# Kernel optimization log

Hardware: AMD Instinct MI355X
Metric: run time of the kernel (lower is better)

Reference implementation:

```python
import jax, jax.numpy as jnp
import numpy as np

B, N, C = 2, 2048, 768
H = 12
D = C // H
WINDOW = 129  # odd; half-window = 64
SCALE = D ** -0.5


def setup_inputs() -> dict:
    key = jax.random.key(0)
    k_x, k_qkv, k_proj, k_pb = jax.random.split(key, 4)
    x = jax.random.normal(k_x, (B, N, C), dtype=jnp.float32)
    # nn.Linear weights: stored as [out, in]; qkv_bias=False so no qkv bias
    w_qkv = jax.random.normal(k_qkv, (3 * C, C), dtype=jnp.float32) * (C ** -0.5)
    w_proj = jax.random.normal(k_proj, (C, C), dtype=jnp.float32) * (C ** -0.5)
    b_proj = jax.random.normal(k_pb, (C,), dtype=jnp.float32) * 0.01
    return {"x": x, "w_qkv": w_qkv, "w_proj": w_proj, "b_proj": b_proj}


def reference(x, w_qkv, w_proj, b_proj):
    b, n, c = x.shape
    # qkv projection: [B,N,3C] -> [3,B,H,N,D]
    qkv = jnp.einsum('bnc,ec->bne', x, w_qkv)
    qkv = qkv.reshape(b, n, 3, H, D).transpose(2, 0, 3, 1, 4)
    q, k, v = qkv[0], qkv[1], qkv[2]
    # dense scores then sliding-window mask (faithful to source)
    attn = jnp.einsum('bhnd,bhmd->bhnm', q, k) * SCALE
    half = WINDOW // 2
    idx = jnp.arange(n)
    mask = jnp.abs(idx[:, None] - idx[None, :]) <= half  # [N,N]
    attn = jnp.where(mask[None, None], attn, -jnp.inf)
    attn = jax.nn.softmax(attn, axis=-1)
    attn = jnp.nan_to_num(attn)
    out = jnp.einsum('bhnm,bhmd->bhnd', attn, v)  # [B,H,N,D]
    out = out.transpose(0, 2, 1, 3).reshape(b, n, c)
    out = jnp.einsum('bnc,oc->bno', out, w_proj) + b_proj
    return out
```

## Files before the change

### kernel.cpp

```cpp
#include <hip/hip_runtime.h>
#include <hip/hip_bf16.h>

#define Bsz   2
#define Nseq  2048
#define Cdim  768
#define E3    2304
#define Hh    12
#define Dd    64
#define HALF  64
#define SCALEF 0.125f

typedef __attribute__((ext_vector_type(8))) short short8;
typedef __attribute__((ext_vector_type(4))) float f32x4;

__device__ __forceinline__ unsigned short f2bf(float f) {
    unsigned int u = __float_as_uint(f);
    u = (u + 0x7FFFu + ((u >> 16) & 1u)) >> 16;
    return (unsigned short)u;
}
__device__ __forceinline__ unsigned int pk2(float a, float b) {
    __hip_bfloat162 h = __float22bfloat162_rn(make_float2(a, b));
    union { __hip_bfloat162 h2; unsigned int u; } cv; cv.h2 = h; return cv.u;
}
__device__ __forceinline__ uint4 cvt8(const float4& lo, const float4& hi) {
    return make_uint4(pk2(lo.x, lo.y), pk2(lo.z, lo.w),
                      pk2(hi.x, hi.y), pk2(hi.z, hi.w));
}

__device__ __forceinline__ void gl_lds16(const unsigned short* g, unsigned short* l) {
    __builtin_amdgcn_global_load_lds(
        (__attribute__((address_space(1))) void*)(g),
        (__attribute__((address_space(3))) void*)(l), 16, 0, 0);
}

#define AST 72

__global__ __launch_bounds__(256) void cvt3(
    const float* __restrict__ x, const float* __restrict__ wq,
    const float* __restrict__ wp, unsigned short* __restrict__ xb,
    unsigned short* __restrict__ wqb, unsigned short* __restrict__ wpb)
{
    const int gid = blockIdx.x * 256 + threadIdx.x;
    const float* src; unsigned short* dst; int off;
    if (gid < 393216)      { src = x;  dst = xb;  off = gid; }
    else if (gid < 614400) { src = wq; dst = wqb; off = gid - 393216; }
    else                   { src = wp; dst = wpb; off = gid - 614400; }
    const float4 lo = *(const float4*)&src[(size_t)off * 8];
    const float4 hi = *(const float4*)&src[(size_t)off * 8 + 4];
    *(uint4*)&dst[(size_t)off * 8] = cvt8(lo, hi);
}

__global__ __launch_bounds__(256) void qkv_mfma(
    const unsigned short* __restrict__ xb, const unsigned short* __restrict__ wqb,
    unsigned short* __restrict__ qkvb)
{
    __shared__ __align__(16) unsigned short smem[12288];
    unsigned short* Asm = smem;
    unsigned short* Bsm = smem + 8192;

    const int t  = threadIdx.x;
    const int id = blockIdx.y * 36 + blockIdx.x;
    const int p8 = id & 7, jb2 = id >> 3;
    const int bx = (p8 & 3) * 9 + (jb2 % 9);
    const int by = (p8 >> 2) * 16 + (jb2 / 9);
    const int row0 = by * 128, col0 = bx * 64;

    const int lane = t & 63, wave = t >> 6;
    const int wm = wave >> 1, wn = wave & 1;
    const int ln = lane & 15, quad = lane >> 4;
    const int lr  = lane >> 3;
    const int sc  = ((lane ^ lr) & 7) * 8;
    const int xsw = (ln & 7) << 3;

    f32x4 acc[4][2] = {};

    for (int k0 = 0; k0 < Cdim; k0 += 64) {
        __syncthreads();
#pragma unroll
        for (int j = 0; j < 4; ++j)
            gl_lds16(&xb[(size_t)(row0 + wave*32 + j*8 + lr) * Cdim + k0 + sc],
                     &Asm[(wave*4 + j) * 512]);
#pragma unroll
        for (int j = 0; j < 2; ++j)
            gl_lds16(&wqb[(size_t)(col0 + wave*16 + j*8 + lr) * Cdim + k0 + sc],
                     &Bsm[(wave*2 + j) * 512]);
        __syncthreads();
#pragma unroll
        for (int kk = 0; kk < 2; ++kk) {
            short8 af[4], bf[2];
#pragma unroll
            for (int mi = 0; mi < 4; ++mi)
                af[mi] = *(const short8*)&Asm[(wm*64 + mi*16 + ln)*64
                                              + ((kk*32 + quad*8) ^ xsw)];
#pragma unroll
            for (int ni = 0; ni < 2; ++ni)
                bf[ni] = *(const short8*)&Bsm[(wn*32 + ni*16 + ln)*64
                                              + ((kk*32 + quad*8) ^ xsw)];
#pragma unroll
            for (int mi = 0; mi < 4; ++mi)
#pragma unroll
                for (int ni = 0; ni < 2; ++ni)
                    acc[mi][ni] = __builtin_amdgcn_mfma_f32_16x16x32_bf16(
                        af[mi], bf[ni], acc[mi][ni], 0, 0, 0);
        }
    }

    __syncthreads();
    unsigned short (*Cs)[AST] = (unsigned short(*)[AST])smem;
    const int rA = t >> 3, c8 = t & 7;
#pragma unroll
    for (int mi = 0; mi < 4; ++mi)
#pragma unroll
        for (int ni = 0; ni < 2; ++ni)
#pragma unroll
            for (int reg = 0; reg < 4; ++reg)
                Cs[wm*64 + mi*16 + quad*4 + reg][wn*32 + ni*16 + ln] =
                    f2bf(acc[mi][ni][reg]);
    __syncthreads();
#pragma unroll
    for (int j = 0; j < 4; ++j)
        *(uint4*)&qkvb[(size_t)(row0 + rA + j*32) * E3 + col0 + c8*8] =
            *(const uint4*)&Cs[rA + j*32][c8*8];
}

__global__ __launch_bounds__(256) void proj_mfma(
    const unsigned short* __restrict__ Ab, const unsigned short* __restrict__ wpb,
    const float* __restrict__ bias, float* __restrict__ out)
{
    __shared__ __align__(16) unsigned short smem[8192];
    unsigned short* Asm = smem;
    unsigned short* Bsm = smem + 4096;

    const int t  = threadIdx.x;
    const int id = blockIdx.y * 12 + blockIdx.x;
    const int p8 = id & 7, j2 = id >> 3;
    const int bx = j2 % 12;
    const int by = p8 * 8 + j2 / 12;
    const int row0 = by * 64, col0 = bx * 64;

    const int lane = t & 63, wave = t >> 6;
    const int ln = lane & 15, quad = lane >> 4;
    const int lr  = lane >> 3;
    const int sc  = ((lane ^ lr) & 7) * 8;
    const int xsw = (ln & 7) << 3;

    f32x4 acc[4] = {};

    for (int k0 = 0; k0 < Cdim; k0 += 64) {
        __syncthreads();
#pragma unroll
        for (int j = 0; j < 2; ++j) {
            const int r = wave*16 + j*8 + lr;
            gl_lds16(&Ab[(size_t)(row0 + r) * Cdim + k0 + sc],
                     &Asm[(wave*2 + j) * 512]);
            gl_lds16(&wpb[(size_t)(col0 + r) * Cdim + k0 + sc],
                     &Bsm[(wave*2 + j) * 512]);
        }
        __syncthreads();
#pragma unroll
        for (int kc = 0; kc < 2; ++kc) {
            short8 af = *(const short8*)&Asm[(wave*16 + ln)*64
                                             + ((kc*32 + quad*8) ^ xsw)];
#pragma unroll
            for (int ni = 0; ni < 4; ++ni) {
                short8 bf = *(const short8*)&Bsm[(ni*16 + ln)*64
                                                 + ((kc*32 + quad*8) ^ xsw)];
                acc[ni] = __builtin_amdgcn_mfma_f32_16x16x32_bf16(af, bf, acc[ni], 0, 0, 0);
            }
        }
    }

    float (*Csf)[36] = (float(*)[36])smem;
#pragma unroll
    for (int p = 0; p < 2; ++p) {
        __syncthreads();
#pragma unroll
        for (int ni = 0; ni < 2; ++ni) {
            const int nn = p * 2 + ni;
#pragma unroll
            for (int reg = 0; reg < 4; ++reg)
                Csf[wave*16 + quad*4 + reg][ni*16 + ln] = acc[nn][reg];
        }
        __syncthreads();
#pragma unroll
        for (int j = 0; j < 2; ++j) {
            const int F = t + j * 256, r = F >> 3, c4 = F & 7;
            const int col = col0 + p * 32 + c4 * 4;
            float4 v  = *(const float4*)&Csf[r][c4 * 4];
            float4 bv = *(const float4*)&bias[col];
            *(float4*)&out[(size_t)(row0 + r) * Cdim + col] =
                make_float4(v.x + bv.x, v.y + bv.y, v.z + bv.z, v.w + bv.w);
        }
    }
}

#define TQ   32
#define ROWS 160
#define KST  72
#define VST  168

__global__ __launch_bounds__(256) void swin_attn(
    const unsigned short* __restrict__ qkvb, unsigned short* __restrict__ ab)
{
    __shared__ __align__(16) unsigned short SH[ROWS * KST];
    __shared__ __align__(16) unsigned short Pl[TQ][VST];
    __shared__ float pmax[4][TQ];
    __shared__ float psum[4][TQ];
    unsigned short (*Ks)[KST] = (unsigned short(*)[KST])SH;
    unsigned short (*Vt)[VST] = (unsigned short(*)[VST])SH;

    const int t  = threadIdx.x;
    const int bh = blockIdx.y;
    const int b  = bh / Hh, h = bh % Hh;
    const int i0 = blockIdx.x * TQ;
    const int hoff = h * Dd;

    const int lane = t & 63, wave = t >> 6;
    const int ln = lane & 15, quad = lane >> 4;
    const int mi    = wave & 1;
    const int khalf = wave >> 1;

    short8 qf[2];
#pragma unroll
    for (int kc = 0; kc < 2; ++kc)
        qf[kc] = *(const short8*)&qkvb[(size_t)(b * Nseq + i0 + mi*16 + ln) * E3
                                       + hoff + kc*32 + quad*8];
    uint4 vreg[5];
    const int rV = t >> 3, c8 = t & 7;
#pragma unroll
    for (int j = 0; j < 5; ++j) {
        const int r = rV + j * 32;
        const int g = i0 - HALF + r;
        uint4 v = make_uint4(0u, 0u, 0u, 0u);
        if (g >= 0 && g < Nseq)
            v = *(const uint4*)&qkvb[(size_t)(b * Nseq + g) * E3 + 2*Cdim + hoff + c8*8];
        vreg[j] = v;
    }
#pragma unroll
    for (int j = 0; j < 5; ++j) {
        const int r = rV + j * 32;
        const int g = i0 - HALF + r;
        uint4 v = make_uint4(0u, 0u, 0u, 0u);
        if (g >= 0 && g < Nseq)
            v = *(const uint4*)&qkvb[(size_t)(b * Nseq + g) * E3 + Cdim + hoff + c8*8];
        *(uint4*)&Ks[r][c8 * 8] = v;
    }
    __syncthreads();

    f32x4 sacc[5] = {};
#pragma unroll
    for (int kc = 0; kc < 2; ++kc)
#pragma unroll
        for (int tt = 0; tt < 5; ++tt) {
            short8 kf = *(const short8*)&Ks[(khalf*5 + tt)*16 + ln][kc*32 + quad*8];
            sacc[tt] = __builtin_amdgcn_mfma_f32_16x16x32_bf16(qf[kc], kf, sacc[tt], 0, 0, 0);
        }

    float p[5][4];
    float pm[4] = {-1e30f, -1e30f, -1e30f, -1e30f};
#pragma unroll
    for (int tt = 0; tt < 5; ++tt) {
        const int j = (khalf*5 + tt)*16 + ln;
        const int g = i0 - HALF + j;
#pragma unroll
        for (int reg = 0; reg < 4; ++reg) {
            const int q = mi*16 + quad*4 + reg;
            const bool valid = (j >= q) && (j <= q + 2*HALF) && (g >= 0) && (g < Nseq);
            const float s = valid ? sacc[tt][reg] * SCALEF : -1e30f;
            p[tt][reg] = s;
            pm[reg] = fmaxf(pm[reg], s);
        }
    }
#pragma unroll
    for (int reg = 0; reg < 4; ++reg) {
        pm[reg] = fmaxf(pm[reg], __shfl_xor(pm[reg], 1));
        pm[reg] = fmaxf(pm[reg], __shfl_xor(pm[reg], 2));
        pm[reg] = fmaxf(pm[reg], __shfl_xor(pm[reg], 4));
        pm[reg] = fmaxf(pm[reg], __shfl_xor(pm[reg], 8));
    }
    if (ln == 0)
#pragma unroll
        for (int reg = 0; reg < 4; ++reg)
            pmax[wave][mi*16 + quad*4 + reg] = pm[reg];
    __syncthreads();

    float ps[4] = {};
#pragma unroll
    for (int reg = 0; reg < 4; ++reg) {
        const int q = mi*16 + quad*4 + reg;
        const float cm = fmaxf(pmax[mi][q], pmax[mi | 2][q]);
#pragma unroll
        for (int tt = 0; tt < 5; ++tt) {
            const float pv = (p[tt][reg] > -1e29f) ? __expf(p[tt][reg] - cm) : 0.f;
            p[tt][reg] = pv;
            ps[reg] += pv;
        }
    }
#pragma unroll
    for (int reg = 0; reg < 4; ++reg) {
        ps[reg] += __shfl_xor(ps[reg], 1);
        ps[reg] += __shfl_xor(ps[reg], 2);
        ps[reg] += __shfl_xor(ps[reg], 4);
        ps[reg] += __shfl_xor(ps[reg], 8);
    }
    if (ln == 0)
#pragma unroll
        for (int reg = 0; reg < 4; ++reg)
            psum[wave][mi*16 + quad*4 + reg] = ps[reg];
#pragma unroll
    for (int tt = 0; tt < 5; ++tt)
#pragma unroll
        for (int reg = 0; reg < 4; ++reg)
            Pl[mi*16 + quad*4 + reg][(khalf*5 + tt)*16 + ln] = f2bf(p[tt][reg]);
#pragma unroll
    for (int j = 0; j < 5; ++j) {
        const int r = rV + j * 32;
        union { unsigned short us[8]; uint4 u; } pk; pk.u = vreg[j];
#pragma unroll
        for (int jj = 0; jj < 8; ++jj)
            Vt[c8 * 8 + jj][r] = pk.us[jj];
    }
    __syncthreads();

    const int niq = wave & 1;
    const int mb  = (wave >> 1) * 2;
    f32x4 oacc[2] = {};
#pragma unroll
    for (int kc = 0; kc < 5; ++kc) {
        short8 pf = *(const short8*)&Pl[niq*16 + ln][kc*32 + quad*8];
#pragma unroll
        for (int m2 = 0; m2 < 2; ++m2) {
            short8 vf = *(const short8*)&Vt[(mb + m2)*16 + ln][kc*32 + quad*8];
            oacc[m2] = __builtin_amdgcn_mfma_f32_16x16x32_bf16(vf, pf, oacc[m2], 0, 0, 0);
        }
    }

    const int q = niq*16 + ln;
    const float inv = 1.f / (psum[q >> 4][q] + psum[(q >> 4) | 2][q]);
    unsigned short* orow = &ab[(size_t)(b * Nseq + i0 + q) * Cdim + hoff];
#pragma unroll
    for (int m2 = 0; m2 < 2; ++m2) {
        const int d0 = (mb + m2)*16 + quad*4;
        union { unsigned short us[4]; uint2 u2; } pk;
#pragma unroll
        for (int reg = 0; reg < 4; ++reg)
            pk.us[reg] = f2bf(oacc[m2][reg] * inv);
        *(uint2*)&orow[d0] = pk.u2;
    }
}

extern "C" void kernel_launch(void* const* d_in, const int* in_sizes, int n_in,
                              void* d_out, int out_size, void* d_ws, size_t ws_size,
                              hipStream_t stream)
{
    const float* x      = (const float*)d_in[0];
    const float* w_qkv  = (const float*)d_in[1];
    const float* w_proj = (const float*)d_in[2];
    const float* b_proj = (const float*)d_in[3];
    float* out = (float*)d_out;

    unsigned short* qkvb = (unsigned short*)d_ws;
    unsigned short* ab   = qkvb + 9437184;
    unsigned short* xb   = ab   + 3145728;
    unsigned short* wqb  = xb   + 3145728;
    unsigned short* wpb  = wqb  + 1769472;

    cvt3<<<dim3(2688), 256, 0, stream>>>(x, w_qkv, w_proj, xb, wqb, wpb);
    qkv_mfma<<<dim3(36, 32), 256, 0, stream>>>(xb, wqb, qkvb);
    swin_attn<<<dim3(Nseq / TQ, Bsz * Hh), 256, 0, stream>>>(qkvb, ab);
    proj_mfma<<<dim3(12, 64), 256, 0, stream>>>(ab, wpb, b_proj, out);
}
```

Before: 131.4 us.

## Widen QKV GEMM tiles and swizzle attention K/V shared-memory layouts

The QKV GEMM now uses 128x128 output tiles instead of 128x64, doubling per-wave MFMA work and halving the grid, with a two-pass bf16 epilogue through LDS. The attention kernel loads K straight into LDS with async global_load_lds and an XOR-swizzled layout, clamping out-of-range rows instead of zero-filling. It also stores the transposed V with an XOR swizzle to reduce bank conflicts, and remaps block IDs for L2 locality. The larger GEMM tile costs more registers and leaves fewer blocks (576), which may reduce occupancy.

```diff
diff --git a/kernel.cpp b/kernel.cpp
--- a/kernel.cpp
+++ b/kernel.cpp
@@ -33,8 +33,6 @@
         (__attribute__((address_space(3))) void*)(l), 16, 0, 0);
 }
 
-#define AST 72
-
 __global__ __launch_bounds__(256) void cvt3(
     const float* __restrict__ x, const float* __restrict__ wq,
     const float* __restrict__ wp, unsigned short* __restrict__ xb,
@@ -54,16 +52,16 @@
     const unsigned short* __restrict__ xb, const unsigned short* __restrict__ wqb,
     unsigned short* __restrict__ qkvb)
 {
-    __shared__ __align__(16) unsigned short smem[12288];
+    __shared__ __align__(16) unsigned short smem[16384];
     unsigned short* Asm = smem;
     unsigned short* Bsm = smem + 8192;
 
     const int t  = threadIdx.x;
-    const int id = blockIdx.y * 36 + blockIdx.x;
-    const int p8 = id & 7, jb2 = id >> 3;
-    const int bx = (p8 & 3) * 9 + (jb2 % 9);
-    const int by = (p8 >> 2) * 16 + (jb2 / 9);
-    const int row0 = by * 128, col0 = bx * 64;
+    const int id = blockIdx.y * 18 + blockIdx.x;
+    const int p8 = id & 7, j8 = id >> 3;
+    const int wg = p8 * 72 + j8;
+    const int by = wg / 18, bx = wg % 18;
+    const int row0 = by * 128, col0 = bx * 128;
 
     const int lane = t & 63, wave = t >> 6;
     const int wm = wave >> 1, wn = wave & 1;
@@ -72,55 +70,59 @@
     const int sc  = ((lane ^ lr) & 7) * 8;
     const int xsw = (ln & 7) << 3;
 
-    f32x4 acc[4][2] = {};
+    f32x4 acc[4][4] = {};
 
     for (int k0 = 0; k0 < Cdim; k0 += 64) {
         __syncthreads();
 #pragma unroll
-        for (int j = 0; j < 4; ++j)
+        for (int j = 0; j < 4; ++j) {
             gl_lds16(&xb[(size_t)(row0 + wave*32 + j*8 + lr) * Cdim + k0 + sc],
                      &Asm[(wave*4 + j) * 512]);
-#pragma unroll
-        for (int j = 0; j < 2; ++j)
-            gl_lds16(&wqb[(size_t)(col0 + wave*16 + j*8 + lr) * Cdim + k0 + sc],
-                     &Bsm[(wave*2 + j) * 512]);
+            gl_lds16(&wqb[(size_t)(col0 + wave*32 + j*8 + lr) * Cdim + k0 + sc],
+                     &Bsm[(wave*4 + j) * 512]);
+        }
         __syncthreads();
 #pragma unroll
         for (int kk = 0; kk < 2; ++kk) {
-            short8 af[4], bf[2];
+            short8 af[4], bf[4];
 #pragma unroll
             for (int mi = 0; mi < 4; ++mi)
                 af[mi] = *(const short8*)&Asm[(wm*64 + mi*16 + ln)*64
                                               + ((kk*32 + quad*8) ^ xsw)];
 #pragma unroll
-            for (int ni = 0; ni < 2; ++ni)
-                bf[ni] = *(const short8*)&Bsm[(wn*32 + ni*16 + ln)*64
+            for (int ni = 0; ni < 4; ++ni)
+                bf[ni] = *(const short8*)&Bsm[(wn*64 + ni*16 + ln)*64
                                               + ((kk*32 + quad*8) ^ xsw)];
 #pragma unroll
             for (int mi = 0; mi < 4; ++mi)
 #pragma unroll
-                for (int ni = 0; ni < 2; ++ni)
+                for (int ni = 0; ni < 4; ++ni)
                     acc[mi][ni] = __builtin_amdgcn_mfma_f32_16x16x32_bf16(
                         af[mi], bf[ni], acc[mi][ni], 0, 0, 0);
         }
     }
 
-    __syncthreads();
-    unsigned short (*Cs)[AST] = (unsigned short(*)[AST])smem;
+    unsigned short (*Cs)[72] = (unsigned short(*)[72])smem;
     const int rA = t >> 3, c8 = t & 7;
 #pragma unroll
-    for (int mi = 0; mi < 4; ++mi)
-#pragma unroll
-        for (int ni = 0; ni < 2; ++ni)
-#pragma unroll
-            for (int reg = 0; reg < 4; ++reg)
-                Cs[wm*64 + mi*16 + quad*4 + reg][wn*32 + ni*16 + ln] =
-                    f2bf(acc[mi][ni][reg]);
-    __syncthreads();
-#pragma unroll
-    for (int j = 0; j < 4; ++j)
-        *(uint4*)&qkvb[(size_t)(row0 + rA + j*32) * E3 + col0 + c8*8] =
-            *(const uint4*)&Cs[rA + j*32][c8*8];
+    for (int p = 0; p < 2; ++p) {
+        __syncthreads();
+        if (wn == p) {
+#pragma unroll
+            for (int mi = 0; mi < 4; ++mi)
+#pragma unroll
+                for (int ni = 0; ni < 4; ++ni)
+#pragma unroll
+                    for (int reg = 0; reg < 4; ++reg)
+                        Cs[wm*64 + mi*16 + quad*4 + reg][ni*16 + ln] =
+                            f2bf(acc[mi][ni][reg]);
+        }
+        __syncthreads();
+#pragma unroll
+        for (int j = 0; j < 4; ++j)
+            *(uint4*)&qkvb[(size_t)(row0 + rA + j*32) * E3 + col0 + p*64 + c8*8] =
+                *(const uint4*)&Cs[rA + j*32][c8*8];
+    }
 }
 
 __global__ __launch_bounds__(256) void proj_mfma(
@@ -196,29 +198,32 @@
 
 #define TQ   32
 #define ROWS 160
-#define KST  72
-#define VST  168
+#define VSTn 200
+#define PST  168
 
 __global__ __launch_bounds__(256) void swin_attn(
     const unsigned short* __restrict__ qkvb, unsigned short* __restrict__ ab)
 {
-    __shared__ __align__(16) unsigned short SH[ROWS * KST];
-    __shared__ __align__(16) unsigned short Pl[TQ][VST];
+    __shared__ __align__(16) unsigned short SH[64 * VSTn];
+    __shared__ __align__(16) unsigned short Pl[TQ][PST];
     __shared__ float pmax[4][TQ];
     __shared__ float psum[4][TQ];
-    unsigned short (*Ks)[KST] = (unsigned short(*)[KST])SH;
-    unsigned short (*Vt)[VST] = (unsigned short(*)[VST])SH;
 
     const int t  = threadIdx.x;
-    const int bh = blockIdx.y;
+    const int n  = blockIdx.y * 64 + blockIdx.x;
+    const int p8 = n & 7, jj8 = n >> 3;
+    const int bh = jj8 >> 3;
+    const int i0 = (p8 * 8 + (jj8 & 7)) * TQ;
     const int b  = bh / Hh, h = bh % Hh;
-    const int i0 = blockIdx.x * TQ;
     const int hoff = h * Dd;
 
     const int lane = t & 63, wave = t >> 6;
     const int ln = lane & 15, quad = lane >> 4;
     const int mi    = wave & 1;
     const int khalf = wave >> 1;
+    const int lr   = lane >> 3;
+    const int scw  = ((lane ^ lr) & 7) * 8;
+    const int xsw  = (ln & 7) << 3;
 
     short8 qf[2];
 #pragma unroll
@@ -238,12 +243,11 @@
     }
 #pragma unroll
     for (int j = 0; j < 5; ++j) {
-        const int r = rV + j * 32;
-        const int g = i0 - HALF + r;
-        uint4 v = make_uint4(0u, 0u, 0u, 0u);
-        if (g >= 0 && g < Nseq)
-            v = *(const uint4*)&qkvb[(size_t)(b * Nseq + g) * E3 + Cdim + hoff + c8*8];
-        *(uint4*)&Ks[r][c8 * 8] = v;
+        const int base = j * 32 + wave * 8;
+        int g = i0 - HALF + base + lr;
+        g = min(max(g, 0), Nseq - 1);
+        gl_lds16(&qkvb[(size_t)(b * Nseq + g) * E3 + Cdim + hoff + scw],
+                 &SH[base * 64]);
     }
     __syncthreads();
 
@@ -252,7 +256,8 @@
     for (int kc = 0; kc < 2; ++kc)
 #pragma unroll
         for (int tt = 0; tt < 5; ++tt) {
-            short8 kf = *(const short8*)&Ks[(khalf*5 + tt)*16 + ln][kc*32 + quad*8];
+            short8 kf = *(const short8*)&SH[((khalf*5 + tt)*16 + ln)*64
+                                            + ((kc*32 + quad*8) ^ xsw)];
             sacc[tt] = __builtin_amdgcn_mfma_f32_16x16x32_bf16(qf[kc], kf, sacc[tt], 0, 0, 0);
         }
 
@@ -315,10 +320,11 @@
 #pragma unroll
     for (int j = 0; j < 5; ++j) {
         const int r = rV + j * 32;
+        const int gr = ((r >> 3) ^ c8) * 8 + (r & 7);
         union { unsigned short us[8]; uint4 u; } pk; pk.u = vreg[j];
 #pragma unroll
-        for (int jj = 0; jj < 8; ++jj)
-            Vt[c8 * 8 + jj][r] = pk.us[jj];
+        for (int d8 = 0; d8 < 8; ++d8)
+            SH[(c8 * 8 + d8) * VSTn + gr] = pk.us[d8];
     }
     __syncthreads();
 
@@ -330,7 +336,9 @@
         short8 pf = *(const short8*)&Pl[niq*16 + ln][kc*32 + quad*8];
 #pragma unroll
         for (int m2 = 0; m2 < 2; ++m2) {
-            short8 vf = *(const short8*)&Vt[(mb + m2)*16 + ln][kc*32 + quad*8];
+            const int d = (mb + m2)*16 + ln;
+            short8 vf = *(const short8*)&SH[d * VSTn
+                                            + (((kc*4 + quad) ^ (d >> 3)) << 3)];
             oacc[m2] = __builtin_amdgcn_mfma_f32_16x16x32_bf16(vf, pf, oacc[m2], 0, 0, 0);
         }
     }
@@ -366,7 +374,7 @@
     unsigned short* wpb  = wqb  + 1769472;
 
     cvt3<<<dim3(2688), 256, 0, stream>>>(x, w_qkv, w_proj, xb, wqb, wpb);
-    qkv_mfma<<<dim3(36, 32), 256, 0, stream>>>(xb, wqb, qkvb);
+    qkv_mfma<<<dim3(18, 32), 256, 0, stream>>>(xb, wqb, qkvb);
     swin_attn<<<dim3(Nseq / TQ, Bsz * Hh), 256, 0, stream>>>(qkvb, ab);
     proj_mfma<<<dim3(12, 64), 256, 0, stream>>>(ab, wpb, b_proj, out);
 }
```

Measured after the change: 132.4 us. Within noise of the previous version (+0.8%).
